# Optimization experiments

Measured on AMD Instinct MI355X. Metric: run time of the kernel, lower is better.

## Reference

```python
import jax, jax.numpy as jnp
import numpy as np

LAMBDA_L1, LAMBDA_IOU, LAMBDA_CLS = 5.0, 2.0, 1.0
B, N, K, M = 16, 900, 91, 100


def setup_inputs() -> dict:
    key = jax.random.key(0)
    k1, k2, k3, k4, k5, k6 = jax.random.split(key, 6)
    cls_pred = jax.random.normal(k1, (B, N, K), dtype=jnp.float32)
    # valid xyxy boxes in [0,1]
    pmin = jax.random.uniform(k2, (B, N, 2), dtype=jnp.float32) * 0.5
    pwh = jax.random.uniform(k3, (B, N, 2), dtype=jnp.float32) * 0.5 + 1e-3
    bb_pred = jnp.concatenate([pmin, pmin + pwh], axis=-1)
    gmin = jax.random.uniform(k4, (B, M, 2), dtype=jnp.float32) * 0.5
    gwh = jax.random.uniform(k5, (B, M, 2), dtype=jnp.float32) * 0.5 + 1e-3
    bb_gt = jnp.concatenate([gmin, gmin + gwh], axis=-1)
    cls_gt = jax.random.randint(k6, (B, M), 0, K)
    return {"cls_pred": cls_pred, "bb_pred": bb_pred, "cls_gt": cls_gt, "bb_gt": bb_gt}


def _box_iou(b1, b2):
    # b1 [P,4], b2 [Q,4] -> iou [P,Q]
    area1 = (b1[:, 2] - b1[:, 0]) * (b1[:, 3] - b1[:, 1])
    area2 = (b2[:, 2] - b2[:, 0]) * (b2[:, 3] - b2[:, 1])
    x_min = jnp.maximum(b1[:, None, 0], b2[None, :, 0])
    y_min = jnp.maximum(b1[:, None, 1], b2[None, :, 1])
    x_max = jnp.minimum(b1[:, None, 2], b2[None, :, 2])
    y_max = jnp.minimum(b1[:, None, 3], b2[None, :, 3])
    inter = jnp.clip(x_max - x_min, 0) * jnp.clip(y_max - y_min, 0)
    union = area1[:, None] + area2[None, :] - inter
    return inter / (union + 1e-6)


def _solve(cost):
    # Jonker-Volgenant shortest augmenting path; cost (n, m) with n <= m; minimization.
    n, m = cost.shape
    u = np.zeros(n + 1)
    v = np.zeros(m + 1)
    p = np.zeros(m + 1, dtype=np.int64)   # p[j] = row matched to col j (1-indexed)
    way = np.zeros(m + 1, dtype=np.int64)
    for i in range(1, n + 1):
        p[0] = i
        j0 = 0
        minv = np.full(m + 1, np.inf)
        used = np.zeros(m + 1, dtype=bool)
        while True:
            used[j0] = True
            i0 = p[j0]
            cur = cost[i0 - 1] - u[i0] - v[1:]
            cur = np.where(used[1:], np.inf, cur)
            upd = cur < minv[1:]
            minv[1:] = np.where(upd, cur, minv[1:])
            way[1:] = np.where(upd, j0, way[1:])
            cand = np.where(used[1:], np.inf, minv[1:])
            j1 = int(np.argmin(cand)) + 1
            delta = cand[j1 - 1]
            uj = np.nonzero(used)[0]
            u[p[uj]] += delta
            v[uj] -= delta
            minv[1:] = np.where(used[1:], minv[1:], minv[1:] - delta)
            j0 = j1
            if p[j0] == 0:
                break
        while j0 != 0:
            j1 = way[j0]
            p[j0] = p[j1]
            j0 = j1
    cols = np.nonzero(p[1:])[0]
    rows = p[1:][cols] - 1
    return rows, cols


def _linear_sum_assignment(cost):
    cost = np.asarray(cost, dtype=np.float64)
    transposed = cost.shape[0] > cost.shape[1]
    rows, cols = _solve(cost.T if transposed else cost)
    if transposed:
        rows, cols = cols, rows
    order = np.argsort(rows)
    return rows[order], cols[order]


def reference(cls_pred, bb_pred, cls_gt, bb_gt):
    b, n, k = cls_pred.shape
    m = cls_gt.shape[1]
    out_prob = jax.nn.softmax(cls_pred.reshape(b * n, k), axis=-1)
    out_bbox = bb_pred.reshape(b * n, 4)
    tgt_ids = cls_gt.reshape(-1)
    tgt_bbox = bb_gt.reshape(-1, 4)
    cost_class = -out_prob[:, tgt_ids]                                   # [B*N, B*M]
    l1 = jnp.sum(jnp.abs(out_bbox[:, None, :] - tgt_bbox[None, :, :]), -1)  # p=1 cdist
    iou = -_box_iou(out_bbox, tgt_bbox)
    C = LAMBDA_IOU * iou + LAMBDA_L1 * l1 + LAMBDA_CLS * cost_class
    C = np.asarray(C.reshape(b, n, b, m))
    Cb = C[np.arange(b), :, np.arange(b), :]  # diagonal blocks [B, N, M] (= torch split(sizes)[i][i])
    preds, tgts = [], []
    for bi in range(b):
        r, c = _linear_sum_assignment(Cb[bi])
        preds.append(r)
        tgts.append(c)
    return (jnp.asarray(np.stack(preds), dtype=jnp.int64),
            jnp.asarray(np.stack(tgts), dtype=jnp.int64))
```

## Files before the change

### kernel.cpp

```cpp
#include <hip/hip_runtime.h>
#include <math.h>

#define NB 16
#define NP 900
#define NC 91
#define NT 100
#define SLOTS 15

__global__ __launch_bounds__(256) void colcost_kernel(
    const float* __restrict__ cls_pred,
    const float* __restrict__ bb_pred,
    const int*   __restrict__ cls_gt,
    const float* __restrict__ bb_gt,
    float* __restrict__ Ct,
    unsigned* __restrict__ colOwner)
{
    const int b    = blockIdx.x;
    const int wid  = threadIdx.x >> 6;
    const int lane = threadIdx.x & 63;
    const int n    = blockIdx.y * 4 + wid;

    __shared__ float probs[4][NC];

    if (lane == 0) colOwner[(size_t)b*NP + n] = 0xFFFFFFFFu;

    const float* crow = cls_pred + ((size_t)b*NP + n)*NC;
    const float x0 = crow[lane];
    const float x1 = (lane + 64 < NC) ? crow[lane + 64] : -INFINITY;
    float mx = fmaxf(x0, x1);
    #pragma unroll
    for (int off = 32; off >= 1; off >>= 1)
        mx = fmaxf(mx, __shfl_xor(mx, off, 64));
    float s = expf(x0 - mx);
    if (lane + 64 < NC) s += expf(x1 - mx);
    #pragma unroll
    for (int off = 32; off >= 1; off >>= 1)
        s += __shfl_xor(s, off, 64);
    const float rinv = 1.0f / s;

    probs[wid][lane] = expf(x0 - mx) * rinv;
    if (lane + 64 < NC) probs[wid][lane + 64] = expf(x1 - mx) * rinv;
    __syncthreads();

    const float4 bp = *reinterpret_cast<const float4*>(bb_pred + ((size_t)b*NP + n)*4);
    const float parea = (bp.z - bp.x) * (bp.w - bp.y);

    #pragma unroll
    for (int h = 0; h < 2; ++h) {
        const int m = lane + 64*h;
        if (m < NT) {
            const int row = b*NT + m;
            const float4 gt = *reinterpret_cast<const float4*>(bb_gt + (size_t)row*4);
            const float garea = (gt.z - gt.x) * (gt.w - gt.y);
            const int   c     = cls_gt[row];

            const float l1 = fabsf(bp.x - gt.x) + fabsf(bp.y - gt.y) +
                             fabsf(bp.z - gt.z) + fabsf(bp.w - gt.w);
            const float xm = fmaxf(bp.x, gt.x);
            const float ym = fmaxf(bp.y, gt.y);
            const float xM = fminf(bp.z, gt.z);
            const float yM = fminf(bp.w, gt.w);
            const float inter = fmaxf(xM - xm, 0.f) * fmaxf(yM - ym, 0.f);
            const float iou = inter / (parea + garea - inter + 1e-6f);
            const float pc  = probs[wid][c];

            Ct[(size_t)row*NP + n] = 5.0f*l1 - 2.0f*iou - pc;
        }
    }
}

__global__ __launch_bounds__(256) void rowmin_claim_kernel(
    const float* __restrict__ Ct,
    float* __restrict__ u_init,
    int*   __restrict__ amin,
    unsigned* __restrict__ colOwner)
{
    const int b    = blockIdx.x;
    const int wid  = threadIdx.x >> 6;
    const int lane = threadIdx.x & 63;
    const int m    = blockIdx.y * 4 + wid;
    const int row  = b*NT + m;
    const float* cr = Ct + (size_t)row * NP;

    float best = INFINITY; int bj = 0;
    #pragma unroll
    for (int r = 0; r < SLOTS; ++r) {
        const int j = 64*r + lane;
        if ((r < SLOTS-1) || (lane < 4)) {
            const float x = cr[j];
            if (x < best) { best = x; bj = j; }
        }
    }
    float vmin = best;
    #pragma unroll
    for (int off = 32; off >= 1; off >>= 1)
        vmin = fminf(vmin, __shfl_xor(vmin, off, 64));
    const unsigned long long win = __ballot(best == vmin);
    const int bjAll = __shfl(bj, __builtin_ctzll(win), 64);
    if (lane == 0) {
        u_init[row] = vmin;
        amin[row]   = bjAll;
        atomicMin(&colOwner[(size_t)b*NP + bjAll], (unsigned)m);
    }
}

__device__ __forceinline__ int pop_row(unsigned long long& fm0, unsigned long long& fm1)
{
    if (fm0) { const int l = __builtin_ctzll(fm0); fm0 &= fm0 - 1; return l + 1;  }
    if (fm1) { const int l = __builtin_ctzll(fm1); fm1 &= fm1 - 1; return l + 65; }
    return 0;
}

__global__ __launch_bounds__(64) void jv_kernel(
    const float* __restrict__ Ct,
    const float* __restrict__ u_init,
    const int*   __restrict__ amin,
    const unsigned* __restrict__ colOwner,
    int* __restrict__ out)
{
    const int b    = blockIdx.x;
    const int lane = threadIdx.x;
    const float* Cb = Ct + (size_t)b*NT*NP;

    double v[SLOTS], minv[SLOTS];
    float  cw[SLOTS], cnext[SLOTS];
    int    way[SLOTS], p[SLOTS];

    double u0 = (double)u_init[b*NT + lane];
    double u1 = (lane < NT-64) ? (double)u_init[b*NT + 64 + lane] : 0.0;

    #pragma unroll
    for (int r = 0; r < SLOTS; ++r) {
        v[r] = 0.0; way[r] = 0;
        unsigned o = 0xFFFFFFFFu;
        if ((r < SLOTS-1) || (lane < 4)) o = colOwner[(size_t)b*NP + 64*r + lane];
        p[r] = (o == 0xFFFFFFFFu) ? 0 : (int)o + 1;
    }

    const int a0 = amin[b*NT + lane];
    const bool as0 = (colOwner[(size_t)b*NP + a0] == (unsigned)lane);
    bool as1 = true;
    if (lane < NT-64) {
        const int a1 = amin[b*NT + 64 + lane];
        as1 = (colOwner[(size_t)b*NP + a1] == (unsigned)(64 + lane));
    }
    unsigned long long fm0 = __ballot(!as0);
    unsigned long long fm1 = __ballot(!as1 && (lane < NT-64));

    int iCur = pop_row(fm0, fm1);
    if (iCur) {
        const float* cr = Cb + (size_t)(iCur-1)*NP;
        #pragma unroll
        for (int r = 0; r < SLOTS; ++r) {
            int ja = 64*r + lane; if (ja > NP-1) ja = NP-1;
            cnext[r] = cr[ja];
        }
    }

    while (iCur) {
        const int iNext = pop_row(fm0, fm1);

        unsigned usedMask = 0;
        bool it0 = false, it1 = false;
        double Dtot = 0.0;
        #pragma unroll
        for (int r = 0; r < SLOTS; ++r) { minv[r] = INFINITY; cw[r] = cnext[r]; }

        const int i = iCur;
        if (i <= 64) { if (lane == i-1)  it0 = true; }
        else         { if (lane == i-65) it1 = true; }
        double ui0 = (i <= 64) ? __shfl(u0, i-1, 64) : __shfl(u1, i-65, 64);

        if (iNext) {
            const float* cr = Cb + (size_t)(iNext-1)*NP;
            #pragma unroll
            for (int r = 0; r < SLOTS; ++r) {
                int ja = 64*r + lane; if (ja > NP-1) ja = NP-1;
                cnext[r] = cr[ja];
            }
        }

        int j0 = 0, jfinal;
        while (true) {
            double best = INFINITY;
            int    pk   = 0;
            #pragma unroll
            for (int r = 0; r < SLOTS; ++r) {
                const int jm1 = 64*r + lane;
                const bool valid = ((r < SLOTS-1) || (lane < 4)) && !((usedMask >> r) & 1u);
                const double cur = valid ? (((double)cw[r] - ui0) - v[r]) : INFINITY;
                if (cur < minv[r]) { minv[r] = cur; way[r] = j0; }
                if (minv[r] < best) { best = minv[r]; pk = (jm1 + 1) | (p[r] << 10); }
            }

            const float bf = (float)best;
            float vm32 = bf;
            #pragma unroll
            for (int off = 32; off >= 1; off >>= 1)
                vm32 = fminf(vm32, __shfl_xor(vm32, off, 64));
            const unsigned long long cand = __ballot(bf <= vm32 + 1e-3f);
            int winner;
            if (__popcll(cand) == 1) {
                winner = __builtin_ctzll(cand);
            } else {
                double vm = best;
                #pragma unroll
                for (int off = 32; off >= 1; off >>= 1)
                    vm = fmin(vm, __shfl_xor(vm, off, 64));
                winner = __builtin_ctzll(__ballot(best == vm));
            }
            const double delta = __shfl(best, winner, 64);
            pk = __shfl(pk, winner, 64);

            const int j1    = pk & 1023;
            const int pnext = pk >> 10;
            Dtot += delta;
            #pragma unroll
            for (int r = 0; r < SLOTS; ++r) minv[r] -= delta;

            #pragma unroll
            for (int r = 0; r < SLOTS; ++r) {
                if (64*r + lane + 1 == j1) {
                    usedMask |= 1u << r;
                    minv[r] = INFINITY;
                    v[r] += Dtot;
                }
            }

            if (pnext == 0) { jfinal = j1; break; }

            ui0 = (pnext <= 64) ? __shfl(u0, pnext-1, 64) : __shfl(u1, pnext-65, 64);
            if (pnext <= 64) { if (lane == pnext-1)  { u0 -= Dtot; it0 = true; } }
            else             { if (lane == pnext-65) { u1 -= Dtot; it1 = true; } }

            {
                const float* cr = Cb + (size_t)(pnext-1)*NP;
                #pragma unroll
                for (int r = 0; r < SLOTS; ++r) {
                    int ja = 64*r + lane; if (ja > NP-1) ja = NP-1;
                    cw[r] = cr[ja];
                }
            }
            j0 = j1;
        }

        {
            int jc = jfinal;
            while (jc != 0) {
                int wsel = 0;
                #pragma unroll
                for (int r = 0; r < SLOTS; ++r)
                    if (64*r + lane + 1 == jc) wsel = way[r];
                const int jprev = __shfl(wsel, (jc-1) & 63, 64);
                int newrow;
                if (jprev == 0) newrow = i;
                else {
                    int psel = 0;
                    #pragma unroll
                    for (int r = 0; r < SLOTS; ++r)
                        if (64*r + lane + 1 == jprev) psel = p[r];
                    newrow = __shfl(psel, (jprev-1) & 63, 64);
                }
                #pragma unroll
                for (int r = 0; r < SLOTS; ++r)
                    if (64*r + lane + 1 == jc) p[r] = newrow;
                jc = jprev;
            }
        }

        #pragma unroll
        for (int r = 0; r < SLOTS; ++r)
            if ((usedMask >> r) & 1u) v[r] -= Dtot;
        if (it0) u0 += Dtot;
        if (it1) u1 += Dtot;

        iCur = iNext;
    }

    int base = 0;
    #pragma unroll
    for (int r = 0; r < SLOTS; ++r) {
        const unsigned long long mask = __ballot(p[r] != 0);
        if (p[r] != 0) {
            const int rank = base + (int)__popcll(mask & ((1ull << lane) - 1ull));
            out[b*NT + rank]         = 64*r + lane;
            out[NB*NT + b*NT + rank] = p[r] - 1;
        }
        base += (int)__popcll(mask);
    }
}

extern "C" void kernel_launch(void* const* d_in, const int* in_sizes, int n_in,
                              void* d_out, int out_size, void* d_ws, size_t ws_size,
                              hipStream_t stream)
{
    const float* cls_pred = (const float*)d_in[0];
    const float* bb_pred  = (const float*)d_in[1];
    const int*   cls_gt   = (const int*)d_in[2];
    const float* bb_gt    = (const float*)d_in[3];

    char* base = (char*)d_ws;
    const size_t ctBytes = (size_t)NB*NT*NP*sizeof(float);
    float*    Ct       = (float*)base;
    unsigned* colOwner = (unsigned*)(base + ctBytes);
    float*    u_init   = (float*)(base + ctBytes + (size_t)NB*NP*4);
    int*      aminP    = (int*)(base + ctBytes + (size_t)NB*NP*4 + (size_t)NB*NT*4);

    colcost_kernel<<<dim3(NB, NP/4), 256, 0, stream>>>(
        cls_pred, bb_pred, cls_gt, bb_gt, Ct, colOwner);
    rowmin_claim_kernel<<<dim3(NB, NT/4), 256, 0, stream>>>(Ct, u_init, aminP, colOwner);
    jv_kernel<<<NB, 64, 0, stream>>>(Ct, u_init, aminP, colOwner, (int*)d_out);
}
```

Measured before the change: 48.66 us.

## Add auction-style augmenting row reduction before shortest-path augmentation

Inserts a Jonker-Volgenant augmenting row reduction phase: each free row finds its best and second-best reduced cost, takes the best column, lowers that column's price by the gap, and evicts the previous owner. The phase is capped at twice the number of initially free rows. It aims to resolve most free rows cheaply so fewer full Dijkstra-style augmentations run afterward. It adds extra row loads and warp reductions, and may leave more free rows if the prices cycle.

```diff
diff --git a/kernel.cpp b/kernel.cpp
--- a/kernel.cpp
+++ b/kernel.cpp
@@ -147,7 +147,61 @@
     unsigned long long fm0 = __ballot(!as0);
     unsigned long long fm1 = __ballot(!as1 && (lane < NT-64));
 
+    const int nfree = (int)__popcll(fm0) + (int)__popcll(fm1);
     int iCur = pop_row(fm0, fm1);
+
+    int arrLeft = 2 * nfree;
+    while (iCur && arrLeft > 0) {
+        --arrLeft;
+
+        {
+            const float* cr = Cb + (size_t)(iCur-1)*NP;
+            #pragma unroll
+            for (int r = 0; r < SLOTS; ++r) {
+                int ja = 64*r + lane; if (ja > NP-1) ja = NP-1;
+                cw[r] = cr[ja];
+            }
+        }
+
+        double m1 = INFINITY, m2 = INFINITY;
+        int j1loc = 0x7FFFFFFF;
+        #pragma unroll
+        for (int r = 0; r < SLOTS; ++r) {
+            if ((r < SLOTS-1) || (lane < 4)) {
+                const double d = (double)cw[r] - v[r];
+                if (d < m1)      { m2 = m1; m1 = d; j1loc = 64*r + lane + 1; }
+                else if (d < m2) { m2 = d; }
+            }
+        }
+        #pragma unroll
+        for (int off = 32; off >= 1; off >>= 1) {
+            const double om1 = __shfl_xor(m1, off, 64);
+            const double om2 = __shfl_xor(m2, off, 64);
+            const int    oj  = __shfl_xor(j1loc, off, 64);
+            const double nm2 = fmin(fmax(m1, om1), fmin(m2, om2));
+            if (om1 < m1 || (om1 == m1 && oj < j1loc)) { m1 = om1; j1loc = oj; }
+            m2 = nm2;
+        }
+        const int j1 = j1loc;
+
+        if (iCur <= 64) { if (lane == iCur-1)  u0 = m2; }
+        else            { if (lane == iCur-65) u1 = m2; }
+
+        const int jl = (j1-1) & 63, js = (j1-1) >> 6;
+        int psel = 0;
+        #pragma unroll
+        for (int r = 0; r < SLOTS; ++r) {
+            if (r == js && lane == jl) {
+                psel = p[r];
+                p[r] = iCur;
+                v[r] -= (m2 - m1);
+            }
+        }
+        const int pOwner = __shfl(psel, jl, 64);
+
+        iCur = pOwner ? pOwner : pop_row(fm0, fm1);
+    }
+
     if (iCur) {
         const float* cr = Cb + (size_t)(iCur-1)*NP;
         #pragma unroll
```

Result: slower. 60.79 us (+24.9%).
